# Optimization experiments

Measured on AMD Instinct MI355X. Metric: run time of the kernel, lower is better.

The kernel has to match this reference:

```python
import jax, jax.numpy as jnp
import numpy as np

B, N, E = 64, 20000, 160000
F_TEXT, HID, OUT = 300, 1024, 1664
NEG_SLOPE = 0.2


def setup_inputs() -> dict:
    key = jax.random.key(0)
    ks = jax.random.split(key, 9)
    img_feat = jax.random.normal(ks[0], (B, OUT), dtype=jnp.float32)
    node_features = jax.random.normal(ks[1], (N, F_TEXT), dtype=jnp.float32)
    edge_src = jax.random.randint(ks[2], (E,), 0, N, dtype=jnp.int32)
    edge_dst = jax.random.randint(ks[3], (E,), 0, N, dtype=jnp.int32)
    edge_weight = jax.random.uniform(ks[4], (E,), dtype=jnp.float32)
    W1 = jax.random.normal(ks[5], (F_TEXT, HID), dtype=jnp.float32) / np.sqrt(F_TEXT)
    b1 = jax.random.normal(ks[6], (HID,), dtype=jnp.float32) * 0.01
    W2 = jax.random.normal(ks[7], (HID, OUT), dtype=jnp.float32) / np.sqrt(HID)
    b2 = jax.random.normal(ks[8], (OUT,), dtype=jnp.float32) * 0.01
    return {"img_feat": img_feat, "node_features": node_features,
            "edge_src": edge_src, "edge_dst": edge_dst, "edge_weight": edge_weight,
            "W1": W1, "b1": b1, "W2": W2, "b2": b2}


def _gcn_norm(edge_src, edge_dst, edge_weight, num_nodes):
    # PyG gcn_norm with add_self_loops=False: symmetric degree normalization
    deg = jax.ops.segment_sum(edge_weight, edge_dst, num_segments=num_nodes)
    dinv = jnp.where(deg > 0, jax.lax.rsqrt(deg), 0.0)
    return dinv[edge_src] * edge_weight * dinv[edge_dst]


def _gcn_conv(x, edge_src, edge_dst, norm, W, b):
    # GCNConv: linear transform, then normalized gather -> scatter-add, then bias
    h = x @ W  # [N, out]
    msgs = h[edge_src] * norm[:, None]  # [E, out] gather + scale
    agg = jax.ops.segment_sum(msgs, edge_dst, num_segments=x.shape[0])
    return agg + b


def reference(img_feat, node_features, edge_src, edge_dst, edge_weight, W1, b1, W2, b2):
    num_nodes = node_features.shape[0]
    norm = _gcn_norm(edge_src, edge_dst, edge_weight, num_nodes)
    x = _gcn_conv(node_features, edge_src, edge_dst, norm, W1, b1)
    x = jnp.where(x >= 0, x, NEG_SLOPE * x)  # leaky_relu(0.2)
    x = _gcn_conv(x, edge_src, edge_dst, norm, W2, b2)
    return img_feat @ x.T  # [B, N]
```

## Files before the change

### kernel.cpp

```cpp
#include <hip/hip_runtime.h>
#include <hip/hip_bf16.h>

#define NNODES 20000
#define NEDGES 160000
#define BQ     64
#define FTEXT  300
#define KPAD1  320
#define HIDDIM 1024
#define OUTDIM 1664

typedef __attribute__((ext_vector_type(8))) short short8;
typedef __attribute__((ext_vector_type(4))) float floatx4;

__device__ inline unsigned short f2bf(float f) {
    union { float f; unsigned int u; } v; v.f = f;
    unsigned int r = v.u + 0x7FFF + ((v.u >> 16) & 1);
    return (unsigned short)(r >> 16);
}
__device__ inline float bf2f(unsigned short h) {
    union { unsigned int u; float f; } v; v.u = ((unsigned int)h) << 16;
    return v.f;
}

__device__ inline void gload16(const unsigned short* g, unsigned short* l) {
    __builtin_amdgcn_global_load_lds(
        (const __attribute__((address_space(1))) unsigned int*)g,
        (__attribute__((address_space(3))) unsigned int*)l, 16, 0, 0);
}

__global__ void degcnt_kernel(const int* __restrict__ dst, const float* __restrict__ w,
                              float* __restrict__ deg, int* __restrict__ cnt, int E) {
    int e = blockIdx.x * blockDim.x + threadIdx.x;
    if (e < E) {
        int d = dst[e];
        atomicAdd(&deg[d], w[e]);
        atomicAdd(&cnt[d], 1);
    }
}

__global__ __launch_bounds__(1024) void scan_kernel(const int* __restrict__ cnt,
                                                    int* __restrict__ row_start, int N) {
    __shared__ int partial[1024];
    const int CH = 20;
    int t = threadIdx.x;
    int begin = t * CH;
    int nloc = N - begin; if (nloc > CH) nloc = CH; if (nloc < 0) nloc = 0;
    int vals[CH];
    int s = 0;
    if (nloc == CH) {
        #pragma unroll
        for (int i = 0; i < CH / 4; i++) {
            int4 v = ((const int4*)(cnt + begin))[i];
            vals[i*4+0] = v.x; vals[i*4+1] = v.y; vals[i*4+2] = v.z; vals[i*4+3] = v.w;
            s += v.x + v.y + v.z + v.w;
        }
    } else {
        for (int i = 0; i < nloc; i++) { vals[i] = cnt[begin + i]; s += vals[i]; }
    }
    partial[t] = s;
    __syncthreads();
    for (int off = 1; off < 1024; off <<= 1) {
        int v = (t >= off) ? partial[t - off] : 0;
        __syncthreads();
        partial[t] += v;
        __syncthreads();
    }
    int run = (t == 0) ? 0 : partial[t - 1];
    for (int i = 0; i < nloc; i++) { row_start[begin + i] = run; run += vals[i]; }
    if (t == 1023) row_start[N] = partial[1023];
}

__global__ void fill_kernel(const int* __restrict__ dst, const int* __restrict__ src,
                            const float* __restrict__ w, const float* __restrict__ deg,
                            const int* __restrict__ row_start, int* __restrict__ cursor,
                            int* __restrict__ src_s, float* __restrict__ wnrm_s, int E) {
    int e = blockIdx.x * blockDim.x + threadIdx.x;
    if (e < E) {
        int d = dst[e], s = src[e];
        float dd = deg[d], ds = deg[s];
        float nv = (ds > 0.f ? rsqrtf(ds) : 0.f) * w[e] * (dd > 0.f ? rsqrtf(dd) : 0.f);
        int pos = row_start[d] + atomicAdd(&cursor[d], 1);
        src_s[pos] = s;
        wnrm_s[pos] = nv;
    }
}

__global__ __launch_bounds__(256) void aggnf_kernel(const unsigned short* __restrict__ nfb,
        const int* __restrict__ row_start, const int* __restrict__ src_s,
        const float* __restrict__ wnrm_s, unsigned short* __restrict__ out) {
    int wave = threadIdx.x >> 6, lane = threadIdx.x & 63;
    int d = blockIdx.x * 4 + wave;
    int s0 = row_start[d], s1 = row_start[d + 1];
    float4 acc  = make_float4(0.f, 0.f, 0.f, 0.f);
    float4 acc2 = make_float4(0.f, 0.f, 0.f, 0.f);
    for (int base = s0; base < s1; base += 64) {
        int m = s1 - base; if (m > 64) m = 64;
        int   src_l = (lane < m) ? src_s[base + lane]  : 0;
        float w_l   = (lane < m) ? wnrm_s[base + lane] : 0.f;
        int sj = __shfl(src_l, 0);
        float wj = __shfl(w_l, 0);
        const ushort4* row = (const ushort4*)(nfb + (long)sj * FTEXT);
        ushort4 hv  = row[lane];
        ushort4 hv2 = make_ushort4(0, 0, 0, 0);
        if (lane < 11) hv2 = row[64 + lane];
        for (int j = 0; j < m; j++) {
            ushort4 nv  = make_ushort4(0, 0, 0, 0);
            ushort4 nv2 = make_ushort4(0, 0, 0, 0);
            float wn = 0.f;
            if (j + 1 < m) {
                int sn = __shfl(src_l, j + 1);
                wn = __shfl(w_l, j + 1);
                const ushort4* nrow = (const ushort4*)(nfb + (long)sn * FTEXT);
                nv = nrow[lane];
                if (lane < 11) nv2 = nrow[64 + lane];
            }
            acc.x  += bf2f(hv.x)  * wj; acc.y  += bf2f(hv.y)  * wj;
            acc.z  += bf2f(hv.z)  * wj; acc.w  += bf2f(hv.w)  * wj;
            acc2.x += bf2f(hv2.x) * wj; acc2.y += bf2f(hv2.y) * wj;
            acc2.z += bf2f(hv2.z) * wj; acc2.w += bf2f(hv2.w) * wj;
            hv = nv; hv2 = nv2; wj = wn;
        }
    }
    unsigned short* orow = out + (long)d * KPAD1;
    ushort4 o;
    o.x = f2bf(acc.x); o.y = f2bf(acc.y); o.z = f2bf(acc.z); o.w = f2bf(acc.w);
    ((ushort4*)orow)[lane] = o;
    if (lane < 16) {
        ushort4 o2 = make_ushort4(0, 0, 0, 0);
        if (lane < 11) {
            o2.x = f2bf(acc2.x); o2.y = f2bf(acc2.y);
            o2.z = f2bf(acc2.z); o2.w = f2bf(acc2.w);
        }
        ((ushort4*)orow)[64 + lane] = o2;
    }
}

#define W1N  (HIDDIM * KPAD1)
#define N1F4 (HIDDIM * OUTDIM / 4)
#define N2F4 (BQ * OUTDIM / 4)
#define N3F4 (NNODES * FTEXT / 4)
__global__ void cvt_all_kernel(const float* __restrict__ W1, unsigned short* __restrict__ W1ch,
                               const float* __restrict__ W2, unsigned short* __restrict__ W2b,
                               const float* __restrict__ img, unsigned short* __restrict__ imgb,
                               const float* __restrict__ nf, unsigned short* __restrict__ nfb) {
    int i = blockIdx.x * 256 + threadIdx.x;
    if (i < W1N) {
        int c   = i >> 13;
        int w   = i & 8191;
        int h   = (w >> 12) & 1;
        int lqg = (w >> 10) & 3;
        int row = (w >> 3) & 127;
        int j   = i & 7;
        int n = (c / 5) * 128 + row;
        int k = (c % 5) * 64 + h * 32 + lqg * 8 + j;
        float v = (k < FTEXT) ? W1[(long)k * HIDDIM + n] : 0.f;
        W1ch[i] = f2bf(v);
        return;
    }
    i -= W1N;
    const float* in; unsigned short* outp; int j;
    if (i < N1F4)                    { in = W2;  outp = W2b;  j = i; }
    else if (i < N1F4 + N2F4)        { in = img; outp = imgb; j = i - N1F4; }
    else if (i < N1F4 + N2F4 + N3F4) { in = nf;  outp = nfb;  j = i - N1F4 - N2F4; }
    else return;
    float4 v = ((const float4*)in)[j];
    ushort4 o;
    o.x = f2bf(v.x); o.y = f2bf(v.y); o.z = f2bf(v.z); o.w = f2bf(v.w);
    ((ushort4*)outp)[j] = o;
}

__global__ __launch_bounds__(256) void ztcvec_kernel(const float* __restrict__ Ztf,
        unsigned short* __restrict__ Zt, const float* __restrict__ img,
        const float* __restrict__ b2, float* __restrict__ cvec) {
    if (blockIdx.x < (BQ * HIDDIM) / 256) {
        int i = blockIdx.x * 256 + threadIdx.x;
        Zt[i] = f2bf(Ztf[i]);
    } else {
        int b = blockIdx.x - (BQ * HIDDIM) / 256;
        int l = threadIdx.x;
        float v = 0.f;
        for (int f = l; f < OUTDIM; f += 256) v += img[(long)b * OUTDIM + f] * b2[f];
        __shared__ float red[256];
        red[l] = v;
        __syncthreads();
        if (l < 64) {
            v = red[l] + red[l + 64] + red[l + 128] + red[l + 192];
            for (int off = 32; off > 0; off >>= 1) v += __shfl_down(v, off);
            if (l == 0) cvec[b] = v;
        }
    }
}

template<int EPI, int OUT_BF16, int ATOMIC, int NT>
__global__ __launch_bounds__(256) void mfma_gemm(
        const unsigned short* __restrict__ A, const unsigned short* __restrict__ B,
        const float* __restrict__ bias, void* __restrict__ Cv,
        int M, int N, int K, int ldc) {
    constexpr int CT = NT / 16;
    __shared__ unsigned short As[128][40];
    __shared__ unsigned short Bs[NT][40];
    int t = threadIdx.x;
    int m0 = blockIdx.y * 128;
    int n0 = blockIdx.x * NT;
    int klen = K / gridDim.z;
    int kbeg = blockIdx.z * klen;
    int wave = t >> 6, lane = t & 63;
    int lm = lane & 15, lq = lane >> 4;
    floatx4 acc[2][CT] = {};
    for (int k0 = kbeg; k0 < kbeg + klen; k0 += 32) {
        #pragma unroll
        for (int p = 0; p < 2; p++) {
            int idx = p * 256 + t;
            int r = idx >> 2, c8 = (idx & 3) * 8;
            uint4 v = make_uint4(0, 0, 0, 0);
            int gm = m0 + r;
            if (gm < M) v = *(const uint4*)(A + (long)gm * K + k0 + c8);
            *(uint4*)&As[r][c8] = v;
        }
        #pragma unroll
        for (int p = 0; p < NT / 64; p++) {
            int idx = p * 256 + t;
            int r = idx >> 2, c8 = (idx & 3) * 8;
            uint4 v = *(const uint4*)(B + (long)(n0 + r) * K + k0 + c8);
            *(uint4*)&Bs[r][c8] = v;
        }
        __syncthreads();
        short8 a[2], b[CT];
        #pragma unroll
        for (int rt = 0; rt < 2; rt++)
            a[rt] = *(const short8*)&As[wave * 32 + rt * 16 + lm][lq * 8];
        #pragma unroll
        for (int ct = 0; ct < CT; ct++)
            b[ct] = *(const short8*)&Bs[ct * 16 + lm][lq * 8];
        #pragma unroll
        for (int rt = 0; rt < 2; rt++)
            #pragma unroll
            for (int ct = 0; ct < CT; ct++)
                acc[rt][ct] = __builtin_amdgcn_mfma_f32_16x16x32_bf16(
                    a[rt], b[ct], acc[rt][ct], 0, 0, 0);
        __syncthreads();
    }
    #pragma unroll
    for (int rt = 0; rt < 2; rt++) {
        #pragma unroll
        for (int r = 0; r < 4; r++) {
            int gm = m0 + wave * 32 + rt * 16 + lq * 4 + r;
            if (gm >= M) continue;
            #pragma unroll
            for (int ct = 0; ct < CT; ct++) {
                int gn = n0 + ct * 16 + lm;
                float v = acc[rt][ct][r];
                if (EPI) { v += bias[gn]; v = v >= 0.f ? v : 0.2f * v; }
                if (OUT_BF16)      ((unsigned short*)Cv)[(long)gm * ldc + gn] = f2bf(v);
                else if (ATOMIC)   atomicAdd((float*)Cv + (long)gm * ldc + gn, v);
                else               ((float*)Cv)[(long)gm * ldc + gn] = v;
            }
        }
    }
}

__global__ __launch_bounds__(640) void xy_gemm(
        const unsigned short* __restrict__ aggNF, const unsigned short* __restrict__ W1ch,
        const float* __restrict__ b1, const unsigned short* __restrict__ Zt,
        float* __restrict__ Y, int M) {
    __shared__ unsigned short Bs[2][8192];
    __shared__ unsigned short xs[80][136];
    float (*ys)[68] = (float (*)[68])xs;
    int t = threadIdx.x;
    int wave = t >> 6, lane = t & 63;
    int lm = lane & 15, lq = lane >> 4;
    int wm = wave >> 1, wn = wave & 1;
    int m0 = blockIdx.x * 80;

    if (t < 512) {
        gload16(W1ch + t * 8, &Bs[0][t * 8]);
        gload16(W1ch + 4096 + t * 8, &Bs[0][4096 + t * 8]);
    }
    short8 afr[10];
    {
        const unsigned short* ap = aggNF + (long)(m0 + wm * 16 + lm) * KPAD1 + lq * 8;
        #pragma unroll
        for (int kk = 0; kk < 10; kk++)
            afr[kk] = *(const short8*)(ap + kk * 32);
    }
    __syncthreads();
    int cur = 0;
    floatx4 yacc[4] = {};
    for (int nt = 0; nt < 8; nt++) {
        floatx4 acc[4] = {};
        for (int s = 0; s < 5; s++) {
            int c = nt * 5 + s + 1;
            if (c < 40 && t < 512) {
                const unsigned short* src = W1ch + (long)c * 8192 + t * 8;
                gload16(src,        &Bs[cur ^ 1][t * 8]);
                gload16(src + 4096, &Bs[cur ^ 1][4096 + t * 8]);
            }
            #pragma unroll
            for (int h = 0; h < 2; h++) {
                short8 a = afr[s * 2 + h];
                #pragma unroll
                for (int ct = 0; ct < 4; ct++) {
                    short8 b = *(const short8*)&Bs[cur][h * 4096 + lq * 1024
                                                        + (wn * 64 + ct * 16 + lm) * 8];
                    acc[ct] = __builtin_amdgcn_mfma_f32_16x16x32_bf16(a, b, acc[ct], 0, 0, 0);
                }
            }
            __syncthreads();
            cur ^= 1;
        }
        #pragma unroll
        for (int ct = 0; ct < 4; ct++) {
            int col = wn * 64 + ct * 16 + lm;
            float bv = b1[nt * 128 + col];
            #pragma unroll
            for (int r = 0; r < 4; r++) {
                float v = acc[ct][r] + bv;
                v = v >= 0.f ? v : 0.2f * v;
                xs[wm * 16 + lq * 4 + r][col] = f2bf(v);
            }
        }
        #pragma unroll
        for (int kk2 = 0; kk2 < 2; kk2++) {
            short8 a = *(const short8*)&xs[wm * 16 + lm][wn * 64 + kk2 * 32 + lq * 8];
            #pragma unroll
            for (int bt = 0; bt < 4; bt++) {
                short8 b = *(const short8*)(Zt + (long)(bt * 16 + lm) * HIDDIM
                                                + nt * 128 + wn * 64 + kk2 * 32 + lq * 8);
                yacc[bt] = __builtin_amdgcn_mfma_f32_16x16x32_bf16(a, b, yacc[bt], 0, 0, 0);
            }
        }
    }
    __syncthreads();
    if (wn == 1) {
        #pragma unroll
        for (int bt = 0; bt < 4; bt++)
            #pragma unroll
            for (int r = 0; r < 4; r++)
                ys[wm * 16 + lq * 4 + r][bt * 16 + lm] = yacc[bt][r];
    }
    __syncthreads();
    if (wn == 0) {
        #pragma unroll
        for (int bt = 0; bt < 4; bt++)
            #pragma unroll
            for (int r = 0; r < 4; r++) {
                int row = wm * 16 + lq * 4 + r;
                Y[(long)(m0 + row) * 64 + bt * 16 + lm]
                    = yacc[bt][r] + ys[row][bt * 16 + lm];
            }
    }
}

__global__ __launch_bounds__(256) void outagg_kernel(const float* __restrict__ Y,
        const int* __restrict__ row_start, const int* __restrict__ src_s,
        const float* __restrict__ wnrm_s, const float* __restrict__ c,
        float* __restrict__ out, int N) {
    __shared__ float tile[4][68];
    int d0 = blockIdx.x * 4;
    int t = threadIdx.x;
    int wave = t >> 6, lane = t & 63;
    int d = d0 + wave;
    int s0 = row_start[d], s1 = row_start[d + 1];
    float acc = 0.f;
    for (int base = s0; base < s1; base += 64) {
        int m = s1 - base; if (m > 64) m = 64;
        int   src_l = (lane < m) ? src_s[base + lane]  : 0;
        float w_l   = (lane < m) ? wnrm_s[base + lane] : 0.f;
        int sj = __shfl(src_l, 0);
        float wj = __shfl(w_l, 0);
        float yv = Y[(long)sj * 64 + lane];
        for (int j = 0; j < m; j++) {
            float yn = 0.f, wn = 0.f;
            if (j + 1 < m) {
                int sn = __shfl(src_l, j + 1);
                wn = __shfl(w_l, j + 1);
                yn = Y[(long)sn * 64 + lane];
            }
            acc += wj * yv;
            yv = yn; wj = wn;
        }
    }
    tile[wave][lane] = acc + c[lane];
    __syncthreads();
    int b = t >> 2, j = t & 3;
    out[(long)b * N + d0 + j] = tile[j][b];
}

extern "C" void kernel_launch(void* const* d_in, const int* in_sizes, int n_in,
                              void* d_out, int out_size, void* d_ws, size_t ws_size,
                              hipStream_t stream) {
    const float* img_feat      = (const float*)d_in[0];
    const float* node_features = (const float*)d_in[1];
    const int*   edge_src      = (const int*)d_in[2];
    const int*   edge_dst      = (const int*)d_in[3];
    const float* edge_weight   = (const float*)d_in[4];
    const float* W1            = (const float*)d_in[5];
    const float* b1            = (const float*)d_in[6];
    const float* W2            = (const float*)d_in[7];
    const float* b2            = (const float*)d_in[8];
    float* out = (float*)d_out;

    const int N = NNODES, E = NEDGES;

    char* ws = (char*)d_ws;
    size_t off = 0;
    auto alloc = [&](size_t bytes) -> void* {
        void* p = ws + off;
        off = (off + bytes + 255) & ~(size_t)255;
        return p;
    };
    float*          deg       = (float*)alloc((size_t)N * 4);
    int*            cnt       = (int*)alloc((size_t)N * 4);
    int*            cursor    = (int*)alloc((size_t)N * 4);
    float*          Ztf       = (float*)alloc((size_t)BQ * HIDDIM * 4);
    size_t zero_bytes = off;
    float*          Y         = (float*)alloc((size_t)N * BQ * 4);
    int*            row_start = (int*)alloc((size_t)(N + 1) * 4);
    int*            src_s     = (int*)alloc((size_t)E * 4);
    float*          wnrm_s    = (float*)alloc((size_t)E * 4);
    unsigned short* aggNF     = (unsigned short*)alloc((size_t)N * KPAD1 * 2);
    unsigned short* W1ch      = (unsigned short*)alloc((size_t)HIDDIM * KPAD1 * 2);
    unsigned short* W2b       = (unsigned short*)alloc((size_t)HIDDIM * OUTDIM * 2);
    unsigned short* imgb      = (unsigned short*)alloc((size_t)BQ * OUTDIM * 2);
    unsigned short* nfb       = (unsigned short*)alloc((size_t)N * FTEXT * 2);
    unsigned short* Zt        = (unsigned short*)alloc((size_t)BQ * HIDDIM * 2);
    float*          cvec      = (float*)alloc((size_t)BQ * 4);

    hipMemsetAsync(ws, 0, zero_bytes, stream);

    int eb = (E + 255) / 256;
    degcnt_kernel<<<eb, 256, 0, stream>>>(edge_dst, edge_weight, deg, cnt, E);
    scan_kernel<<<1, 1024, 0, stream>>>(cnt, row_start, N);
    fill_kernel<<<eb, 256, 0, stream>>>(edge_dst, edge_src, edge_weight, deg, row_start,
                                        cursor, src_s, wnrm_s, E);

    cvt_all_kernel<<<(W1N + (N1F4 + N2F4 + N3F4) + 255) / 256, 256, 0, stream>>>(
        W1, W1ch, W2, W2b, img_feat, imgb, node_features, nfb);

    mfma_gemm<0, 0, 1, 64><<<dim3(HIDDIM / 64, 1, 13), 256, 0, stream>>>(
        imgb, W2b, nullptr, Ztf, BQ, HIDDIM, OUTDIM, HIDDIM);
    ztcvec_kernel<<<(BQ * HIDDIM) / 256 + BQ, 256, 0, stream>>>(Ztf, Zt, img_feat, b2, cvec);

    aggnf_kernel<<<N / 4, 256, 0, stream>>>(nfb, row_start, src_s, wnrm_s, aggNF);

    xy_gemm<<<dim3(NNODES / 80), 640, 0, stream>>>(aggNF, W1ch, b1, Zt, Y, N);

    outagg_kernel<<<N / 4, 256, 0, stream>>>(Y, row_start, src_s, wnrm_s, cvec, out, N);
}
```

Baseline: 233.2 us.

## Restructure xy_gemm into smaller blocks with 5-stage W1 prefetch ring

```diff
diff --git a/kernel.cpp b/kernel.cpp
--- a/kernel.cpp
+++ b/kernel.cpp
@@ -145,14 +145,14 @@
                                const float* __restrict__ nf, unsigned short* __restrict__ nfb) {
     int i = blockIdx.x * 256 + threadIdx.x;
     if (i < W1N) {
-        int c   = i >> 13;
-        int w   = i & 8191;
-        int h   = (w >> 12) & 1;
-        int lqg = (w >> 10) & 3;
+        int c   = i >> 12;
+        int w   = i & 4095;
+        int lqg = w >> 10;
         int row = (w >> 3) & 127;
         int j   = i & 7;
-        int n = (c / 5) * 128 + row;
-        int k = (c % 5) * 64 + h * 32 + lqg * 8 + j;
+        int nt = c / 10, s = c - nt * 10;
+        int n = nt * 128 + row;
+        int k = s * 32 + lqg * 8 + j;
         float v = (k < FTEXT) ? W1[(long)k * HIDDIM + n] : 0.f;
         W1ch[i] = f2bf(v);
         return;
@@ -259,23 +259,19 @@
     }
 }
 
-__global__ __launch_bounds__(640) void xy_gemm(
+__global__ __launch_bounds__(256, 3) void xy_gemm(
         const unsigned short* __restrict__ aggNF, const unsigned short* __restrict__ W1ch,
         const float* __restrict__ b1, const unsigned short* __restrict__ Zt,
         float* __restrict__ Y, int M) {
-    __shared__ unsigned short Bs[2][8192];
-    __shared__ unsigned short xs[80][136];
+    __shared__ unsigned short Bs[5][4096];
+    __shared__ unsigned short xs[32][136];
     float (*ys)[68] = (float (*)[68])xs;
     int t = threadIdx.x;
     int wave = t >> 6, lane = t & 63;
     int lm = lane & 15, lq = lane >> 4;
     int wm = wave >> 1, wn = wave & 1;
-    int m0 = blockIdx.x * 80;
-
-    if (t < 512) {
-        gload16(W1ch + t * 8, &Bs[0][t * 8]);
-        gload16(W1ch + 4096 + t * 8, &Bs[0][4096 + t * 8]);
-    }
+    int m0 = blockIdx.x * 32;
+
     short8 afr[10];
     {
         const unsigned short* ap = aggNF + (long)(m0 + wm * 16 + lm) * KPAD1 + lq * 8;
@@ -283,30 +279,35 @@
         for (int kk = 0; kk < 10; kk++)
             afr[kk] = *(const short8*)(ap + kk * 32);
     }
-    __syncthreads();
-    int cur = 0;
+    #pragma unroll
+    for (int c = 0; c < 3; c++) {
+        const unsigned short* src = W1ch + (long)c * 4096 + t * 8;
+        gload16(src,        &Bs[c][t * 8]);
+        gload16(src + 2048, &Bs[c][2048 + t * 8]);
+    }
+    int cur = 0, nxt = 3;
     floatx4 yacc[4] = {};
     for (int nt = 0; nt < 8; nt++) {
         floatx4 acc[4] = {};
-        for (int s = 0; s < 5; s++) {
-            int c = nt * 5 + s + 1;
-            if (c < 40 && t < 512) {
-                const unsigned short* src = W1ch + (long)c * 8192 + t * 8;
-                gload16(src,        &Bs[cur ^ 1][t * 8]);
-                gload16(src + 4096, &Bs[cur ^ 1][4096 + t * 8]);
-            }
-            #pragma unroll
-            for (int h = 0; h < 2; h++) {
-                short8 a = afr[s * 2 + h];
-                #pragma unroll
-                for (int ct = 0; ct < 4; ct++) {
-                    short8 b = *(const short8*)&Bs[cur][h * 4096 + lq * 1024
-                                                        + (wn * 64 + ct * 16 + lm) * 8];
-                    acc[ct] = __builtin_amdgcn_mfma_f32_16x16x32_bf16(a, b, acc[ct], 0, 0, 0);
-                }
-            }
-            __syncthreads();
-            cur ^= 1;
+        for (int s = 0; s < 10; s++) {
+            int c = nt * 10 + s;
+            {
+                const unsigned short* src = W1ch + (long)(c + 3) * 4096 + t * 8;
+                gload16(src,        &Bs[nxt][t * 8]);
+                gload16(src + 2048, &Bs[nxt][2048 + t * 8]);
+            }
+            asm volatile("s_waitcnt vmcnt(6)" ::: "memory");
+            __builtin_amdgcn_s_barrier();
+            __builtin_amdgcn_sched_barrier(0);
+            short8 a = afr[s];
+            #pragma unroll
+            for (int ct = 0; ct < 4; ct++) {
+                short8 b = *(const short8*)&Bs[cur][lq * 1024
+                                                    + (wn * 64 + ct * 16 + lm) * 8];
+                acc[ct] = __builtin_amdgcn_mfma_f32_16x16x32_bf16(a, b, acc[ct], 0, 0, 0);
+            }
+            cur = (cur + 1 == 5) ? 0 : cur + 1;
+            nxt = (nxt + 1 == 5) ? 0 : nxt + 1;
         }
         #pragma unroll
         for (int ct = 0; ct < 4; ct++) {
@@ -419,7 +420,7 @@
     int*            src_s     = (int*)alloc((size_t)E * 4);
     float*          wnrm_s    = (float*)alloc((size_t)E * 4);
     unsigned short* aggNF     = (unsigned short*)alloc((size_t)N * KPAD1 * 2);
-    unsigned short* W1ch      = (unsigned short*)alloc((size_t)HIDDIM * KPAD1 * 2);
+    unsigned short* W1ch      = (unsigned short*)alloc(((size_t)HIDDIM * KPAD1 + 3 * 4096) * 2);
     unsigned short* W2b       = (unsigned short*)alloc((size_t)HIDDIM * OUTDIM * 2);
     unsigned short* imgb      = (unsigned short*)alloc((size_t)BQ * OUTDIM * 2);
     unsigned short* nfb       = (unsigned short*)alloc((size_t)N * FTEXT * 2);
@@ -443,7 +444,7 @@
 
     aggnf_kernel<<<N / 4, 256, 0, stream>>>(nfb, row_start, src_s, wnrm_s, aggNF);
 
-    xy_gemm<<<dim3(NNODES / 80), 640, 0, stream>>>(aggNF, W1ch, b1, Zt, Y, N);
+    xy_gemm<<<dim3(NNODES / 32), 256, 0, stream>>>(aggNF, W1ch, b1, Zt, Y, N);
 
     outagg_kernel<<<N / 4, 256, 0, stream>>>(Y, row_start, src_s, wnrm_s, cvec, out, N);
 }
```

After: 230.2 us. About the same (-1.3%).
